# Kernel tuning notes

Hardware: AMD Instinct MI355X
Metric: run time of the kernel (lower is better)

The kernel has to match this reference:

```python
import jax, jax.numpy as jnp
import numpy as np

T, N, E, F_IN, H_GNN, H_OUT, RH, G, C = 8, 10000, 160000, 128, 128, 128, 128, 32, 10


def gcn_layer(x, src, dst, W, b):
    # PyG GCNConv: h = D^-1/2 (A+I) D^-1/2 (x W) + b, self-loops added, edge weight 1
    h = x @ W  # [N, H]
    ones = jnp.ones((E,), h.dtype)
    deg = jax.ops.segment_sum(ones, dst, num_segments=N) + 1.0  # +1 for self-loop
    dinv = jax.lax.rsqrt(deg)
    coef = dinv[src] * dinv[dst]  # [E]
    agg = jax.ops.segment_sum(h[src] * coef[:, None], dst, num_segments=N)
    agg = agg + h * (dinv * dinv)[:, None]  # self-loop term
    return agg + b


def snapshot_encode(x, edge_index, batch, W1, b1, W2, b2):
    src, dst = edge_index[0], edge_index[1]
    h = jax.nn.relu(gcn_layer(x, src, dst, W1, b1))
    h = jax.nn.relu(gcn_layer(h, src, dst, W2, b2))
    sums = jax.ops.segment_sum(h, batch, num_segments=G)  # global_mean_pool
    cnts = jax.ops.segment_sum(jnp.ones((N,), h.dtype), batch, num_segments=G)
    return sums / jnp.maximum(cnts, 1.0)[:, None]  # [G, H_OUT]


def gru_layer(seq, Wih, Whh, bih, bhh):
    # seq: [T, G, in]; torch nn.GRU cell equations
    H = Whh.shape[1]

    def step(h, xt):
        gi = xt @ Wih.T + bih
        gh = h @ Whh.T + bhh
        ir, iz, inn = jnp.split(gi, 3, axis=-1)
        hr, hz, hn = jnp.split(gh, 3, axis=-1)
        r = jax.nn.sigmoid(ir + hr)
        z = jax.nn.sigmoid(iz + hz)
        n = jnp.tanh(inn + r * hn)
        h_new = (1.0 - z) * n + z * h
        return h_new, h_new

    h0 = jnp.zeros((seq.shape[1], H), seq.dtype)
    hT, outs = jax.lax.scan(step, h0, seq)
    return outs, hT


def setup_inputs() -> dict:
    key = jax.random.key(0)
    ks = jax.random.split(key, 20)
    s = 0.05
    inp = {
        "x": jax.random.normal(ks[0], (T, N, F_IN), jnp.float32),
        "edge_index": jax.random.randint(ks[1], (T, 2, E), 0, N),
        "batch": jax.random.randint(ks[2], (T, N), 0, G),
        "W1": jax.random.normal(ks[3], (F_IN, H_GNN), jnp.float32) * s,
        "b1": jnp.zeros((H_GNN,), jnp.float32),
        "W2": jax.random.normal(ks[4], (H_GNN, H_OUT), jnp.float32) * s,
        "b2": jnp.zeros((H_OUT,), jnp.float32),
        "Wih0": jax.random.normal(ks[5], (3 * RH, H_OUT), jnp.float32) * s,
        "Whh0": jax.random.normal(ks[6], (3 * RH, RH), jnp.float32) * s,
        "bih0": jnp.zeros((3 * RH,), jnp.float32),
        "bhh0": jnp.zeros((3 * RH,), jnp.float32),
        "Wih1": jax.random.normal(ks[7], (3 * RH, RH), jnp.float32) * s,
        "Whh1": jax.random.normal(ks[8], (3 * RH, RH), jnp.float32) * s,
        "bih1": jnp.zeros((3 * RH,), jnp.float32),
        "bhh1": jnp.zeros((3 * RH,), jnp.float32),
        "Wc": jax.random.normal(ks[9], (C, RH), jnp.float32) * s,
        "bc": jnp.zeros((C,), jnp.float32),
    }
    return inp


def reference(x, edge_index, batch, W1, b1, W2, b2, Wih0, Whh0, bih0, bhh0,
              Wih1, Whh1, bih1, bhh1, Wc, bc):
    # per-snapshot GNN encode, vmapped over T snapshots -> [T, G, H_OUT]
    emb = jax.vmap(snapshot_encode, in_axes=(0, 0, 0, None, None, None, None))(
        x, edge_index, batch, W1, b1, W2, b2)
    outs, _ = gru_layer(emb, Wih0, Whh0, bih0, bhh0)
    _, hT = gru_layer(outs, Wih1, Whh1, bih1, bhh1)  # h_n[-1]: last layer final state
    return hT @ Wc.T + bc  # [G, C]
```

## Files before the change

kernel.cpp:

```cpp
#include <hip/hip_runtime.h>

#define T_ 8
#define N_ 10000
#define E_ 160000
#define G_ 32
#define C_ 10
#define F_ 128

typedef _Float16 f16;
typedef _Float16 f16x2 __attribute__((ext_vector_type(2)));
typedef _Float16 f16x4 __attribute__((ext_vector_type(4)));
typedef _Float16 f16x8 __attribute__((ext_vector_type(8)));
typedef float floatx4 __attribute__((ext_vector_type(4)));

static constexpr size_t ROWS = (size_t)T_ * N_;
static constexpr int SLICE = E_ / 8;

static constexpr size_t OFF_XH    = 0;
static constexpr size_t OFF_A1    = 20480000;
static constexpr size_t OFF_H1    = 40960000;
static constexpr size_t OFF_REC   = 61440000;
static constexpr size_t OFF_CNT   = 66560000;
static constexpr size_t OFF_DINV  = 69120000;
static constexpr size_t OFF_RP    = 69440000;
static constexpr size_t OFF_CNTG  = 69760032;
static constexpr size_t OFF_BRP   = 69761056;
static constexpr size_t OFF_WP    = 69762112;
static constexpr size_t OFF_BLIST = 69827648;
static constexpr size_t OFF_EMBH  = 70147648;
static constexpr size_t OFF_GPACK = 70213184;
static constexpr size_t OFF_GI0   = 70606400;
static constexpr size_t OFF_PART  = 70999616;

__device__ __forceinline__ float sig_fast(float x) {
  return __builtin_amdgcn_rcpf(1.0f + __builtin_amdgcn_exp2f(-1.4426950408889634f * x));
}
__device__ __forceinline__ float tanh_fast(float x) {
  return 1.0f - 2.0f * __builtin_amdgcn_rcpf(1.0f + __builtin_amdgcn_exp2f(2.8853900817779268f * x));
}

__global__ __launch_bounds__(1024) void hist_kernel(const int* __restrict__ ei,
                                                    const int* __restrict__ batch,
                                                    int* __restrict__ cnt,
                                                    int* __restrict__ cntG) {
  __shared__ int hL[N_];
  __shared__ int cL[G_];
  int b = blockIdx.x, tid = threadIdx.x;
  int t = b & 7, s = b >> 3;
  for (int i = tid; i < N_; i += 1024) hL[i] = 0;
  if (tid < G_) cL[tid] = 0;
  __syncthreads();
  const int* dstp = ei + (size_t)t * 2 * E_ + E_ + s * SLICE;
  for (int e4 = tid; e4 < SLICE / 4; e4 += 1024) {
    int4 d = *(const int4*)(dstp + e4 * 4);
    atomicAdd(&hL[d.x], 1); atomicAdd(&hL[d.y], 1);
    atomicAdd(&hL[d.z], 1); atomicAdd(&hL[d.w], 1);
  }
  if (s == 0)
    for (int n = tid; n < N_; n += 1024) atomicAdd(&cL[batch[t * N_ + n]], 1);
  __syncthreads();
  int* cp = cnt + ((size_t)t * 8 + s) * N_;
  for (int i = tid; i < N_; i += 1024) cp[i] = hL[i];
  if (s == 0 && tid < G_) cntG[t * G_ + tid] = cL[tid];
}

__global__ __launch_bounds__(1024) void scan_kernel(int* __restrict__ cnt,
                                                    int* __restrict__ rp,
                                                    float* __restrict__ dinv,
                                                    const int* __restrict__ cntG,
                                                    int* __restrict__ brp) {
  __shared__ int wsum[16];
  __shared__ int carry;
  int t = blockIdx.x, tid = threadIdx.x, lane = tid & 63, wid = tid >> 6;
  if (t == 8) {
    int v = (tid < 256) ? cntG[tid] : 0;
    for (int ofs = 1; ofs < 64; ofs <<= 1) {
      int u = __shfl_up(v, ofs);
      if (lane >= ofs) v += u;
    }
    if (lane == 63 && wid < 4) wsum[wid] = v;
    __syncthreads();
    if (tid < 256) {
      int base = 0;
      for (int w = 0; w < wid; ++w) base += wsum[w];
      if (tid == 0) brp[0] = 0;
      brp[tid + 1] = v + base;
    }
    return;
  }
  if (tid == 0) { carry = 0; rp[t * (N_ + 1)] = 0; }
  __syncthreads();
  for (int c0 = 0; c0 < N_; c0 += 1024) {
    int n = c0 + tid;
    int vs[8];
    int deg = 0;
    if (n < N_) {
#pragma unroll
      for (int s = 0; s < 8; ++s) {
        vs[s] = cnt[((size_t)t * 8 + s) * N_ + n];
        deg += vs[s];
      }
      dinv[t * N_ + n] = rsqrtf((float)deg + 1.0f);
    }
    int v = (n < N_) ? deg : 0;
    int v0 = v;
    for (int ofs = 1; ofs < 64; ofs <<= 1) {
      int u = __shfl_up(v, ofs);
      if (lane >= ofs) v += u;
    }
    if (lane == 63) wsum[wid] = v;
    __syncthreads();
    if (wid == 0) {
      int w = (lane < 16) ? wsum[lane] : 0;
      for (int ofs = 1; ofs < 16; ofs <<= 1) {
        int u = __shfl_up(w, ofs);
        if (lane >= ofs) w += u;
      }
      if (lane < 16) wsum[lane] = w;
    }
    __syncthreads();
    int base = carry + (wid ? wsum[wid - 1] : 0);
    if (n < N_) {
      rp[t * (N_ + 1) + n + 1] = base + v;
      int run = base + v - v0;
#pragma unroll
      for (int s = 0; s < 8; ++s) {
        int vv = vs[s];
        cnt[((size_t)t * 8 + s) * N_ + n] = run;
        run += vv;
      }
    }
    __syncthreads();
    if (tid == 0) carry += wsum[15];
    __syncthreads();
  }
}

__global__ __launch_bounds__(1024) void fill_kernel(const int* __restrict__ ei,
                                                    const int* __restrict__ base,
                                                    int* __restrict__ rec,
                                                    const int* __restrict__ batch,
                                                    const int* __restrict__ brp,
                                                    int* __restrict__ blist) {
  __shared__ int offL[N_];
  __shared__ int cb[G_];
  int b = blockIdx.x, tid = threadIdx.x;
  int t = b & 7, s = b >> 3;
  const int* bp = base + ((size_t)t * 8 + s) * N_;
  for (int i = tid; i < N_; i += 1024) offL[i] = bp[i];
  if (s == 0 && tid < G_) cb[tid] = brp[t * G_ + tid];
  __syncthreads();
  const int* srcp = ei + (size_t)t * 2 * E_ + s * SLICE;
  const int* dstp = srcp + E_;
  int* rt = rec + (size_t)t * E_;
  for (int e4 = tid; e4 < SLICE / 4; e4 += 1024) {
    int4 sv = *(const int4*)(srcp + e4 * 4);
    int4 dv = *(const int4*)(dstp + e4 * 4);
    int p0 = atomicAdd(&offL[dv.x], 1);
    int p1 = atomicAdd(&offL[dv.y], 1);
    int p2 = atomicAdd(&offL[dv.z], 1);
    int p3 = atomicAdd(&offL[dv.w], 1);
    rt[p0] = sv.x; rt[p1] = sv.y; rt[p2] = sv.z; rt[p3] = sv.w;
  }
  if (s == 0) {
    for (int n = tid; n < N_; n += 1024) {
      int g = batch[t * N_ + n];
      int p = atomicAdd(&cb[g], 1);
      blist[p] = t * N_ + n;
    }
  }
}

__global__ void cvt_kernel(const float* __restrict__ x, const float* __restrict__ dinv,
                           f16* __restrict__ xh) {
  size_t i = ((size_t)blockIdx.x * 256 + threadIdx.x) * 4;
  float4 v = *(const float4*)(x + i);
  float d = dinv[i >> 7];
  f16x4 o; o.x = (f16)(v.x * d); o.y = (f16)(v.y * d);
  o.z = (f16)(v.z * d); o.w = (f16)(v.w * d);
  *(f16x4*)(xh + i) = o;
}

__global__ void agg_kernel(const f16* __restrict__ X, f16* __restrict__ A,
                           const int* __restrict__ rp, const int* __restrict__ rec,
                           const float* __restrict__ dinv) {
  int wave = threadIdx.x >> 6, lane = threadIdx.x & 63;
  int b = blockIdx.x;
  int t = b & 7, i = b >> 3;
  int n = i * 4 + wave;
  int row = t * N_ + n;
  float ds = dinv[row];
  f16x2 xv = *(const f16x2*)(X + (size_t)row * F_ + 2 * lane);
  float a00 = (float)xv.x, a01 = (float)xv.y;
  float a10 = 0.f, a11 = 0.f, a20 = 0.f, a21 = 0.f, a30 = 0.f, a31 = 0.f;
  int beg = rp[t * (N_ + 1) + n], end = rp[t * (N_ + 1) + n + 1];
  beg = __builtin_amdgcn_readfirstlane(beg);
  end = __builtin_amdgcn_readfirstlane(end);
  const int* rc = rec + (size_t)t * E_;
  const f16* Xt = X + (size_t)t * N_ * F_;
  int e = beg;
  int i0 = 0, i1 = 0, i2 = 0, i3 = 0;
  if (e + 3 < end) { i0 = rc[e]; i1 = rc[e + 1]; i2 = rc[e + 2]; i3 = rc[e + 3]; }
  for (; e + 7 < end; e += 4) {
    int n0 = rc[e + 4], n1 = rc[e + 5], n2 = rc[e + 6], n3 = rc[e + 7];
    f16x2 h0 = *(const f16x2*)(Xt + (size_t)i0 * F_ + 2 * lane);
    f16x2 h1 = *(const f16x2*)(Xt + (size_t)i1 * F_ + 2 * lane);
    f16x2 h2 = *(const f16x2*)(Xt + (size_t)i2 * F_ + 2 * lane);
    f16x2 h3 = *(const f16x2*)(Xt + (size_t)i3 * F_ + 2 * lane);
    a00 += (float)h0.x; a01 += (float)h0.y;
    a10 += (float)h1.x; a11 += (float)h1.y;
    a20 += (float)h2.x; a21 += (float)h2.y;
    a30 += (float)h3.x; a31 += (float)h3.y;
    i0 = n0; i1 = n1; i2 = n2; i3 = n3;
  }
  if (e + 3 < end) {
    f16x2 h0 = *(const f16x2*)(Xt + (size_t)i0 * F_ + 2 * lane);
    f16x2 h1 = *(const f16x2*)(Xt + (size_t)i1 * F_ + 2 * lane);
    f16x2 h2 = *(const f16x2*)(Xt + (size_t)i2 * F_ + 2 * lane);
    f16x2 h3 = *(const f16x2*)(Xt + (size_t)i3 * F_ + 2 * lane);
    a00 += (float)h0.x; a01 += (float)h0.y;
    a10 += (float)h1.x; a11 += (float)h1.y;
    a20 += (float)h2.x; a21 += (float)h2.y;
    a30 += (float)h3.x; a31 += (float)h3.y;
    e += 4;
  }
  for (; e < end; ++e) {
    int s = rc[e];
    f16x2 hv = *(const f16x2*)(Xt + (size_t)s * F_ + 2 * lane);
    a00 += (float)hv.x; a01 += (float)hv.y;
  }
  float r0 = ds * ((a00 + a10) + (a20 + a30));
  float r1 = ds * ((a01 + a11) + (a21 + a31));
  f16x2 o; o.x = (f16)r0; o.y = (f16)r1;
  *(f16x2*)(A + (size_t)row * F_ + 2 * lane) = o;
}

__global__ void packall_kernel(const float* __restrict__ W1, const float* __restrict__ W2,
                               f16* __restrict__ Wp,
                               const float* __restrict__ A0, const float* __restrict__ A1,
                               const float* __restrict__ A2, const float* __restrict__ A3,
                               f16* __restrict__ gp) {
  int idx = blockIdx.x * 256 + threadIdx.x;
  if (idx < 32768) {
    const float* W = (idx < 16384) ? W1 : W2;
    int l = idx & 16383;
    int j = l & 7, lane = (l >> 3) & 63, ct = (l >> 9) & 7, kc = (l >> 12) & 3;
    int k = kc * 32 + ((lane >> 4) & 3) * 8 + j;
    int n = ct * 16 + (lane & 15);
    Wp[idx] = (f16)W[k * 128 + n];
  } else {
    int gidx = idx - 32768;
    int mat = gidx / 49152, l = gidx - mat * 49152;
    int j = l & 7, lane = (l >> 3) & 63, kc = (l >> 9) & 3, nt = l >> 11;
    int k = kc * 32 + ((lane >> 4) & 3) * 8 + j;
    int u = nt * 16 + (lane & 15);
    const float* W = (mat == 0) ? A0 : (mat == 1) ? A1 : (mat == 2) ? A2 : A3;
    gp[gidx] = (f16)W[u * 128 + k];
  }
}

__global__ __launch_bounds__(256) void gemm_kernel(const f16* __restrict__ A,
                                                   const f16* __restrict__ Wp,
                                                   const float* __restrict__ bias,
                                                   const float* __restrict__ scale,
                                                   f16* __restrict__ O) {
  __shared__ f16x8 Bp[2048];
  const f16x8* Wv = (const f16x8*)Wp;
  for (int i = threadIdx.x; i < 2048; i += 256) Bp[i] = Wv[i];
  __syncthreads();
  int wave = threadIdx.x >> 6, lane = threadIdx.x & 63;
  int quad = lane >> 4, m = lane & 15;
  int rowbase = blockIdx.x * 64 + wave * 16;
  const f16x8* Arow = (const f16x8*)(A + (size_t)(rowbase + m) * F_);
  floatx4 acc[8];
#pragma unroll
  for (int ct = 0; ct < 8; ++ct) { floatx4 z = {0.f, 0.f, 0.f, 0.f}; acc[ct] = z; }
#pragma unroll
  for (int kc = 0; kc < 4; ++kc) {
    f16x8 a = Arow[kc * 4 + quad];
#pragma unroll
    for (int ct = 0; ct < 8; ++ct)
      acc[ct] = __builtin_amdgcn_mfma_f32_16x16x32_f16(a, Bp[(kc * 8 + ct) * 64 + lane],
                                                       acc[ct], 0, 0, 0);
  }
  float sv[4];
#pragma unroll
  for (int r = 0; r < 4; ++r)
    sv[r] = scale ? scale[rowbase + quad * 4 + r] : 1.0f;
#pragma unroll
  for (int ct = 0; ct < 8; ++ct) {
    int colc = ct * 16 + m;
    float bv = bias[colc];
#pragma unroll
    for (int r = 0; r < 4; ++r) {
      int row = rowbase + quad * 4 + r;
      float v = fmaxf(acc[ct][r] + bv, 0.0f) * sv[r];
      O[(size_t)row * F_ + colc] = (f16)v;
    }
  }
}

__global__ void pool1_kernel(const f16* __restrict__ H, const int* __restrict__ brp,
                             const int* __restrict__ blist, float* __restrict__ part) {
  int b = blockIdx.x;
  int wave = threadIdx.x >> 6, lane = threadIdx.x & 63;
  int idx = b >> 1;
  int s = (b & 1) * 4 + wave;
  int beg = brp[idx], end = brp[idx + 1];
  beg = __builtin_amdgcn_readfirstlane(beg);
  end = __builtin_amdgcn_readfirstlane(end);
  int len = end - beg;
  int lo = beg + (int)(((long long)len * s) >> 3);
  int hi = beg + (int)(((long long)len * (s + 1)) >> 3);
  float a00 = 0.f, a01 = 0.f, a10 = 0.f, a11 = 0.f;
  float a20 = 0.f, a21 = 0.f, a30 = 0.f, a31 = 0.f;
  int e = lo;
  for (; e + 3 < hi; e += 4) {
    int r0 = blist[e], r1 = blist[e + 1], r2 = blist[e + 2], r3 = blist[e + 3];
    f16x2 v0 = *(const f16x2*)(H + (size_t)r0 * F_ + 2 * lane);
    f16x2 v1 = *(const f16x2*)(H + (size_t)r1 * F_ + 2 * lane);
    f16x2 v2 = *(const f16x2*)(H + (size_t)r2 * F_ + 2 * lane);
    f16x2 v3 = *(const f16x2*)(H + (size_t)r3 * F_ + 2 * lane);
    a00 += (float)v0.x; a01 += (float)v0.y;
    a10 += (float)v1.x; a11 += (float)v1.y;
    a20 += (float)v2.x; a21 += (float)v2.y;
    a30 += (float)v3.x; a31 += (float)v3.y;
  }
  for (; e < hi; ++e) {
    int r = blist[e];
    f16x2 v = *(const f16x2*)(H + (size_t)r * F_ + 2 * lane);
    a00 += (float)v.x; a01 += (float)v.y;
  }
  float2 o;
  o.x = (a00 + a10) + (a20 + a30);
  o.y = (a01 + a11) + (a21 + a31);
  *(float2*)(part + ((size_t)idx * 8 + s) * F_ + 2 * lane) = o;
}

__global__ void pool2_kernel(const float* __restrict__ part, const int* __restrict__ brp,
                             f16* __restrict__ embh) {
  int idx = blockIdx.x * 2 + (threadIdx.x >> 7);
  int f = threadIdx.x & 127;
  float s = 0.f;
#pragma unroll
  for (int k = 0; k < 8; ++k) s += part[((size_t)idx * 8 + k) * F_ + f];
  int cnt = brp[idx + 1] - brp[idx];
  embh[(size_t)idx * F_ + f] = (f16)(s / fmaxf((float)cnt, 1.0f));
}

__global__ __launch_bounds__(256) void gi0_kernel(const f16* __restrict__ embh,
                                                  const f16* __restrict__ gp,
                                                  float* __restrict__ gi0) {
  int wave = threadIdx.x >> 6, lane = threadIdx.x & 63;
  int quad = lane >> 4, mm = lane & 15;
  int rowbase = blockIdx.x * 64 + wave * 16;
  const f16* Arow = embh + (size_t)(rowbase + mm) * 128;
  floatx4 acc[24];
#pragma unroll
  for (int nt = 0; nt < 24; ++nt) { floatx4 z = {0.f, 0.f, 0.f, 0.f}; acc[nt] = z; }
#pragma unroll
  for (int kc = 0; kc < 4; ++kc) {
    f16x8 a = *(const f16x8*)(Arow + kc * 32 + quad * 8);
#pragma unroll
    for (int nt = 0; nt < 24; ++nt) {
      f16x8 b = *(const f16x8*)(gp + (size_t)(((nt * 4 + kc) * 64 + lane)) * 8);
      acc[nt] = __builtin_amdgcn_mfma_f32_16x16x32_f16(a, b, acc[nt], 0, 0, 0);
    }
  }
#pragma unroll
  for (int nt = 0; nt < 24; ++nt)
#pragma unroll
    for (int r = 0; r < 4; ++r)
      gi0[(size_t)(rowbase + quad * 4 + r) * 384 + nt * 16 + mm] = acc[nt][r];
}

__global__ __launch_bounds__(256, 1) void gru_fused(
    const f16* __restrict__ gp, const float* __restrict__ gi0,
    const float* __restrict__ bih0, const float* __restrict__ bhh0,
    const float* __restrict__ bih1, const float* __restrict__ bhh1,
    const float* __restrict__ Wc, const float* __restrict__ bc,
    float* __restrict__ out) {
  __shared__ f16 hb0[16 * 136];
  __shared__ f16 hb1[16 * 136];
  __shared__ float ghb[2 * 384];
  __shared__ float gib[2 * 384];
  __shared__ float h1s[2 * 128];
  int tid = threadIdx.x, wave = tid >> 6, lane = tid & 63;
  int quad = lane >> 4, mm = lane & 15;
  int g2 = tid >> 7, f = tid & 127;
  int bid = blockIdx.x;

  f16x8 B0[24], B1[24];
#pragma unroll
  for (int i = 0; i < 6; ++i)
#pragma unroll
    for (int kc = 0; kc < 4; ++kc) {
      size_t off = (size_t)((((wave * 6 + i) * 4 + kc) * 64 + lane)) * 8;
      B0[i * 4 + kc] = *(const f16x8*)(gp + 1 * 49152 + off);
      B1[i * 4 + kc] = *(const f16x8*)(gp + 3 * 49152 + off);
    }
  float br0 = bih0[f] + bhh0[f];
  float bz0 = bih0[128 + f] + bhh0[128 + f];
  float bni0 = bih0[256 + f], bnh0 = bhh0[256 + f];
  float br1 = bih1[f] + bhh1[f];
  float bz1 = bih1[128 + f] + bhh1[128 + f];
  float bni1 = bih1[256 + f], bnh1 = bhh1[256 + f];

  for (int i = tid; i < 16 * 136; i += 256) { hb0[i] = (f16)0.f; hb1[i] = (f16)0.f; }
  float h0 = 0.f, h1 = 0.f;
  __syncthreads();

  const f16* wih1 = gp + 2 * 49152;
  for (int t = 0; t < T_; ++t) {
    f16x8 Bs[24];
#pragma unroll
    for (int i = 0; i < 6; ++i)
#pragma unroll
      for (int kc = 0; kc < 4; ++kc)
        Bs[i * 4 + kc] = *(const f16x8*)(wih1 +
            (size_t)((((wave * 6 + i) * 4 + kc) * 64 + lane)) * 8);
    const float* gi = gi0 + (size_t)(t * G_ + bid * 2 + g2) * 384;
    float gir = gi[f], giz = gi[128 + f], gin = gi[256 + f];

    floatx4 acc[6];
#pragma unroll
    for (int i = 0; i < 6; ++i) { floatx4 z = {0.f, 0.f, 0.f, 0.f}; acc[i] = z; }
#pragma unroll
    for (int kc = 0; kc < 4; ++kc) {
      f16x8 a = *(const f16x8*)(hb0 + mm * 136 + kc * 32 + quad * 8);
#pragma unroll
      for (int i = 0; i < 6; ++i)
        acc[i] = __builtin_amdgcn_mfma_f32_16x16x32_f16(a, B0[i * 4 + kc], acc[i], 0, 0, 0);
    }
    if (quad == 0) {
#pragma unroll
      for (int i = 0; i < 6; ++i) {
        ghb[0 * 384 + wave * 96 + i * 16 + mm] = acc[i][0];
        ghb[1 * 384 + wave * 96 + i * 16 + mm] = acc[i][1];
      }
    }
    __syncthreads();

    {
      float hr = ghb[g2 * 384 + f];
      float hz = ghb[g2 * 384 + 128 + f];
      float hn = ghb[g2 * 384 + 256 + f];
      float r = sig_fast(gir + hr + br0);
      float z = sig_fast(giz + hz + bz0);
      float nn = tanh_fast(gin + bni0 + r * (hn + bnh0));
      h0 = (1.0f - z) * nn + z * h0;
      hb0[g2 * 136 + f] = (f16)h0;
    }
    __syncthreads();

    floatx4 accx[6], acch[6];
#pragma unroll
    for (int i = 0; i < 6; ++i) {
      floatx4 z = {0.f, 0.f, 0.f, 0.f}; accx[i] = z; acch[i] = z;
    }
#pragma unroll
    for (int kc = 0; kc < 4; ++kc) {
      f16x8 ax = *(const f16x8*)(hb0 + mm * 136 + kc * 32 + quad * 8);
      f16x8 ah = *(const f16x8*)(hb1 + mm * 136 + kc * 32 + quad * 8);
#pragma unroll
      for (int i = 0; i < 6; ++i) {
        accx[i] = __builtin_amdgcn_mfma_f32_16x16x32_f16(ax, Bs[i * 4 + kc], accx[i], 0, 0, 0);
        acch[i] = __builtin_amdgcn_mfma_f32_16x16x32_f16(ah, B1[i * 4 + kc], acch[i], 0, 0, 0);
      }
    }
    if (quad == 0) {
#pragma unroll
      for (int i = 0; i < 6; ++i) {
        gib[0 * 384 + wave * 96 + i * 16 + mm] = accx[i][0];
        gib[1 * 384 + wave * 96 + i * 16 + mm] = accx[i][1];
        ghb[0 * 384 + wave * 96 + i * 16 + mm] = acch[i][0];
        ghb[1 * 384 + wave * 96 + i * 16 + mm] = acch[i][1];
      }
    }
    __syncthreads();

    {
      float i1r = gib[g2 * 384 + f];
      float i1z = gib[g2 * 384 + 128 + f];
      float i1n = gib[g2 * 384 + 256 + f];
      float hr = ghb[g2 * 384 + f];
      float hz = ghb[g2 * 384 + 128 + f];
      float hn = ghb[g2 * 384 + 256 + f];
      float r = sig_fast(i1r + hr + br1);
      float z = sig_fast(i1z + hz + bz1);
      float nn = tanh_fast(i1n + bni1 + r * (hn + bnh1));
      h1 = (1.0f - z) * nn + z * h1;
      hb1[g2 * 136 + f] = (f16)h1;
    }
    __syncthreads();
  }

  h1s[g2 * 128 + f] = h1;
  __syncthreads();
  if (tid < 2 * C_) {
    int gg = tid / C_, c = tid - gg * C_;
    float s = bc[c];
    const float* wr = Wc + (size_t)c * 128;
    const float* hr = h1s + gg * 128;
    for (int k = 0; k < 128; k += 4) {
      float4 w = *(const float4*)(wr + k);
      s += hr[k] * w.x + hr[k + 1] * w.y + hr[k + 2] * w.z + hr[k + 3] * w.w;
    }
    out[(bid * 2 + gg) * C_ + c] = s;
  }
}

extern "C" void kernel_launch(void* const* d_in, const int* in_sizes, int n_in,
                              void* d_out, int out_size, void* d_ws, size_t ws_size,
                              hipStream_t stream) {
  const float* x    = (const float*)d_in[0];
  const int*   ei   = (const int*)d_in[1];
  const int*   batch= (const int*)d_in[2];
  const float* W1   = (const float*)d_in[3];
  const float* b1   = (const float*)d_in[4];
  const float* W2   = (const float*)d_in[5];
  const float* b2   = (const float*)d_in[6];
  const float* Wih0 = (const float*)d_in[7];
  const float* Whh0 = (const float*)d_in[8];
  const float* bih0 = (const float*)d_in[9];
  const float* bhh0 = (const float*)d_in[10];
  const float* Wih1 = (const float*)d_in[11];
  const float* Whh1 = (const float*)d_in[12];
  const float* bih1 = (const float*)d_in[13];
  const float* bhh1 = (const float*)d_in[14];
  const float* Wc   = (const float*)d_in[15];
  const float* bc   = (const float*)d_in[16];
  float* out = (float*)d_out;

  char* ws = (char*)d_ws;
  f16*   Xh    = (f16*)(ws + OFF_XH);
  f16*   A1    = (f16*)(ws + OFF_A1);
  f16*   H1    = (f16*)(ws + OFF_H1);
  f16*   A2    = A1;
  f16*   H2    = Xh;
  int*   rec   = (int*)(ws + OFF_REC);
  int*   cnt   = (int*)(ws + OFF_CNT);
  float* dinv  = (float*)(ws + OFF_DINV);
  int*   rp    = (int*)(ws + OFF_RP);
  int*   cntG  = (int*)(ws + OFF_CNTG);
  int*   brp   = (int*)(ws + OFF_BRP);
  f16*   Wp    = (f16*)(ws + OFF_WP);
  int*   blist = (int*)(ws + OFF_BLIST);
  f16*   embh  = (f16*)(ws + OFF_EMBH);
  f16*   gp    = (f16*)(ws + OFF_GPACK);
  float* gi0   = (float*)(ws + OFF_GI0);
  float* part  = (float*)(ws + OFF_PART);

  packall_kernel<<<896, 256, 0, stream>>>(W1, W2, Wp, Wih0, Whh0, Wih1, Whh1, gp);
  hist_kernel<<<64, 1024, 0, stream>>>(ei, batch, cnt, cntG);
  scan_kernel<<<9, 1024, 0, stream>>>(cnt, rp, dinv, cntG, brp);
  cvt_kernel<<<10000, 256, 0, stream>>>(x, dinv, Xh);
  fill_kernel<<<64, 1024, 0, stream>>>(ei, cnt, rec, batch, brp, blist);

  agg_kernel<<<20000, 256, 0, stream>>>(Xh, A1, rp, rec, dinv);
  gemm_kernel<<<1250, 256, 0, stream>>>(A1, Wp, b1, dinv, H1);
  agg_kernel<<<20000, 256, 0, stream>>>(H1, A2, rp, rec, dinv);
  gemm_kernel<<<1250, 256, 0, stream>>>(A2, Wp + 16384, b2, (const float*)nullptr, H2);

  pool1_kernel<<<512, 256, 0, stream>>>(H2, brp, blist, part);
  pool2_kernel<<<128, 256, 0, stream>>>(part, brp, embh);
  gi0_kernel<<<4, 256, 0, stream>>>(embh, gp, gi0);
  gru_fused<<<16, 256, 0, stream>>>(gp, gi0, bih0, bhh0, bih1, bhh1, Wc, bc, out);
}
```

Baseline: 309.3 us.

## Fuse neighbor aggregation with the dense GEMM in each GCN layer

Merges the separate agg and gemm kernels into one kernel per layer. Each block first gathers 64 aggregated rows into shared memory, then runs the MFMA GEMM with bias, ReLU and scaling straight from that shared tile. This removes the round-trip of the intermediate aggregated buffer through global memory and drops it from the workspace. In exchange each wave now walks 16 rows one after another with far fewer blocks, and shared memory use per block rises. That can reduce how many gather loads are in flight and lower occupancy.

```diff
diff --git a/kernel.cpp b/kernel.cpp
--- a/kernel.cpp
+++ b/kernel.cpp
@@ -17,20 +17,19 @@
 static constexpr int SLICE = E_ / 8;
 
 static constexpr size_t OFF_XH    = 0;
-static constexpr size_t OFF_A1    = 20480000;
-static constexpr size_t OFF_H1    = 40960000;
-static constexpr size_t OFF_REC   = 61440000;
-static constexpr size_t OFF_CNT   = 66560000;
-static constexpr size_t OFF_DINV  = 69120000;
-static constexpr size_t OFF_RP    = 69440000;
-static constexpr size_t OFF_CNTG  = 69760032;
-static constexpr size_t OFF_BRP   = 69761056;
-static constexpr size_t OFF_WP    = 69762112;
-static constexpr size_t OFF_BLIST = 69827648;
-static constexpr size_t OFF_EMBH  = 70147648;
-static constexpr size_t OFF_GPACK = 70213184;
-static constexpr size_t OFF_GI0   = 70606400;
-static constexpr size_t OFF_PART  = 70999616;
+static constexpr size_t OFF_H1    = 20480000;
+static constexpr size_t OFF_REC   = 40960000;
+static constexpr size_t OFF_CNT   = 46080000;
+static constexpr size_t OFF_DINV  = 48640000;
+static constexpr size_t OFF_RP    = 48960000;
+static constexpr size_t OFF_CNTG  = 49280032;
+static constexpr size_t OFF_BRP   = 49281056;
+static constexpr size_t OFF_WP    = 49282112;
+static constexpr size_t OFF_BLIST = 49347648;
+static constexpr size_t OFF_EMBH  = 49667648;
+static constexpr size_t OFF_GPACK = 49733184;
+static constexpr size_t OFF_GI0   = 50126400;
+static constexpr size_t OFF_PART  = 50519616;
 
 __device__ __forceinline__ float sig_fast(float x) {
   return __builtin_amdgcn_rcpf(1.0f + __builtin_amdgcn_exp2f(-1.4426950408889634f * x));
@@ -181,58 +180,104 @@
   *(f16x4*)(xh + i) = o;
 }
 
-__global__ void agg_kernel(const f16* __restrict__ X, f16* __restrict__ A,
-                           const int* __restrict__ rp, const int* __restrict__ rec,
-                           const float* __restrict__ dinv) {
-  int wave = threadIdx.x >> 6, lane = threadIdx.x & 63;
-  int b = blockIdx.x;
-  int t = b & 7, i = b >> 3;
-  int n = i * 4 + wave;
-  int row = t * N_ + n;
-  float ds = dinv[row];
-  f16x2 xv = *(const f16x2*)(X + (size_t)row * F_ + 2 * lane);
-  float a00 = (float)xv.x, a01 = (float)xv.y;
-  float a10 = 0.f, a11 = 0.f, a20 = 0.f, a21 = 0.f, a30 = 0.f, a31 = 0.f;
-  int beg = rp[t * (N_ + 1) + n], end = rp[t * (N_ + 1) + n + 1];
-  beg = __builtin_amdgcn_readfirstlane(beg);
-  end = __builtin_amdgcn_readfirstlane(end);
+__global__ __launch_bounds__(256) void agg_gemm_kernel(
+    const f16* __restrict__ X, const int* __restrict__ rp, const int* __restrict__ rec,
+    const float* __restrict__ dinv, const f16* __restrict__ Wp,
+    const float* __restrict__ bias, const float* __restrict__ scale,
+    f16* __restrict__ O) {
+  __shared__ f16 At[64 * 136];
+  __shared__ f16x8 Bp[2048];
+  int tid = threadIdx.x, wave = tid >> 6, lane = tid & 63;
+  const f16x8* Wv = (const f16x8*)Wp;
+  for (int i = tid; i < 2048; i += 256) Bp[i] = Wv[i];
+  int b = blockIdx.x, t = b & 7, ib = b >> 3;
+  const int* rpt = rp + t * (N_ + 1);
   const int* rc = rec + (size_t)t * E_;
   const f16* Xt = X + (size_t)t * N_ * F_;
-  int e = beg;
-  int i0 = 0, i1 = 0, i2 = 0, i3 = 0;
-  if (e + 3 < end) { i0 = rc[e]; i1 = rc[e + 1]; i2 = rc[e + 2]; i3 = rc[e + 3]; }
-  for (; e + 7 < end; e += 4) {
-    int n0 = rc[e + 4], n1 = rc[e + 5], n2 = rc[e + 6], n3 = rc[e + 7];
-    f16x2 h0 = *(const f16x2*)(Xt + (size_t)i0 * F_ + 2 * lane);
-    f16x2 h1 = *(const f16x2*)(Xt + (size_t)i1 * F_ + 2 * lane);
-    f16x2 h2 = *(const f16x2*)(Xt + (size_t)i2 * F_ + 2 * lane);
-    f16x2 h3 = *(const f16x2*)(Xt + (size_t)i3 * F_ + 2 * lane);
-    a00 += (float)h0.x; a01 += (float)h0.y;
-    a10 += (float)h1.x; a11 += (float)h1.y;
-    a20 += (float)h2.x; a21 += (float)h2.y;
-    a30 += (float)h3.x; a31 += (float)h3.y;
-    i0 = n0; i1 = n1; i2 = n2; i3 = n3;
-  }
-  if (e + 3 < end) {
-    f16x2 h0 = *(const f16x2*)(Xt + (size_t)i0 * F_ + 2 * lane);
-    f16x2 h1 = *(const f16x2*)(Xt + (size_t)i1 * F_ + 2 * lane);
-    f16x2 h2 = *(const f16x2*)(Xt + (size_t)i2 * F_ + 2 * lane);
-    f16x2 h3 = *(const f16x2*)(Xt + (size_t)i3 * F_ + 2 * lane);
-    a00 += (float)h0.x; a01 += (float)h0.y;
-    a10 += (float)h1.x; a11 += (float)h1.y;
-    a20 += (float)h2.x; a21 += (float)h2.y;
-    a30 += (float)h3.x; a31 += (float)h3.y;
-    e += 4;
-  }
-  for (; e < end; ++e) {
-    int s = rc[e];
-    f16x2 hv = *(const f16x2*)(Xt + (size_t)s * F_ + 2 * lane);
-    a00 += (float)hv.x; a01 += (float)hv.y;
-  }
-  float r0 = ds * ((a00 + a10) + (a20 + a30));
-  float r1 = ds * ((a01 + a11) + (a21 + a31));
-  f16x2 o; o.x = (f16)r0; o.y = (f16)r1;
-  *(f16x2*)(A + (size_t)row * F_ + 2 * lane) = o;
+  for (int m = 0; m < 16; ++m) {
+    int rl = wave * 16 + m;
+    int n = ib * 64 + rl;
+    f16x2 o;
+    if (n < N_) {
+      float ds = dinv[t * N_ + n];
+      f16x2 xv = *(const f16x2*)(Xt + (size_t)n * F_ + 2 * lane);
+      float a00 = (float)xv.x, a01 = (float)xv.y;
+      float a10 = 0.f, a11 = 0.f, a20 = 0.f, a21 = 0.f, a30 = 0.f, a31 = 0.f;
+      int beg = rpt[n], end = rpt[n + 1];
+      beg = __builtin_amdgcn_readfirstlane(beg);
+      end = __builtin_amdgcn_readfirstlane(end);
+      int e = beg;
+      int i0 = 0, i1 = 0, i2 = 0, i3 = 0;
+      if (e + 3 < end) { i0 = rc[e]; i1 = rc[e + 1]; i2 = rc[e + 2]; i3 = rc[e + 3]; }
+      for (; e + 7 < end; e += 4) {
+        int n0 = rc[e + 4], n1 = rc[e + 5], n2 = rc[e + 6], n3 = rc[e + 7];
+        f16x2 h0 = *(const f16x2*)(Xt + (size_t)i0 * F_ + 2 * lane);
+        f16x2 h1 = *(const f16x2*)(Xt + (size_t)i1 * F_ + 2 * lane);
+        f16x2 h2 = *(const f16x2*)(Xt + (size_t)i2 * F_ + 2 * lane);
+        f16x2 h3 = *(const f16x2*)(Xt + (size_t)i3 * F_ + 2 * lane);
+        a00 += (float)h0.x; a01 += (float)h0.y;
+        a10 += (float)h1.x; a11 += (float)h1.y;
+        a20 += (float)h2.x; a21 += (float)h2.y;
+        a30 += (float)h3.x; a31 += (float)h3.y;
+        i0 = n0; i1 = n1; i2 = n2; i3 = n3;
+      }
+      if (e + 3 < end) {
+        f16x2 h0 = *(const f16x2*)(Xt + (size_t)i0 * F_ + 2 * lane);
+        f16x2 h1 = *(const f16x2*)(Xt + (size_t)i1 * F_ + 2 * lane);
+        f16x2 h2 = *(const f16x2*)(Xt + (size_t)i2 * F_ + 2 * lane);
+        f16x2 h3 = *(const f16x2*)(Xt + (size_t)i3 * F_ + 2 * lane);
+        a00 += (float)h0.x; a01 += (float)h0.y;
+        a10 += (float)h1.x; a11 += (float)h1.y;
+        a20 += (float)h2.x; a21 += (float)h2.y;
+        a30 += (float)h3.x; a31 += (float)h3.y;
+        e += 4;
+      }
+      for (; e < end; ++e) {
+        int s = rc[e];
+        f16x2 hv = *(const f16x2*)(Xt + (size_t)s * F_ + 2 * lane);
+        a00 += (float)hv.x; a01 += (float)hv.y;
+      }
+      o.x = (f16)(ds * ((a00 + a10) + (a20 + a30)));
+      o.y = (f16)(ds * ((a01 + a11) + (a21 + a31)));
+    } else {
+      o.x = (f16)0.f; o.y = (f16)0.f;
+    }
+    *(f16x2*)(At + rl * 136 + 2 * lane) = o;
+  }
+  __syncthreads();
+  int quad = lane >> 4, mm = lane & 15;
+  const f16* Arow = At + (wave * 16 + mm) * 136;
+  floatx4 acc[8];
+#pragma unroll
+  for (int ct = 0; ct < 8; ++ct) { floatx4 z = {0.f, 0.f, 0.f, 0.f}; acc[ct] = z; }
+#pragma unroll
+  for (int kc = 0; kc < 4; ++kc) {
+    f16x8 a = *(const f16x8*)(Arow + kc * 32 + quad * 8);
+#pragma unroll
+    for (int ct = 0; ct < 8; ++ct)
+      acc[ct] = __builtin_amdgcn_mfma_f32_16x16x32_f16(a, Bp[(kc * 8 + ct) * 64 + lane],
+                                                       acc[ct], 0, 0, 0);
+  }
+  float sv[4];
+  int nbase = ib * 64 + wave * 16 + quad * 4;
+#pragma unroll
+  for (int r = 0; r < 4; ++r) {
+    int n = nbase + r;
+    sv[r] = (scale && n < N_) ? scale[t * N_ + n] : 1.0f;
+  }
+#pragma unroll
+  for (int ct = 0; ct < 8; ++ct) {
+    int colc = ct * 16 + mm;
+    float bv = bias[colc];
+#pragma unroll
+    for (int r = 0; r < 4; ++r) {
+      int n = nbase + r;
+      if (n < N_) {
+        float v = fmaxf(acc[ct][r] + bv, 0.0f) * sv[r];
+        O[((size_t)t * N_ + n) * F_ + colc] = (f16)v;
+      }
+    }
+  }
 }
 
 __global__ void packall_kernel(const float* __restrict__ W1, const float* __restrict__ W2,
@@ -256,47 +301,6 @@
     int u = nt * 16 + (lane & 15);
     const float* W = (mat == 0) ? A0 : (mat == 1) ? A1 : (mat == 2) ? A2 : A3;
     gp[gidx] = (f16)W[u * 128 + k];
-  }
-}
-
-__global__ __launch_bounds__(256) void gemm_kernel(const f16* __restrict__ A,
-                                                   const f16* __restrict__ Wp,
-                                                   const float* __restrict__ bias,
-                                                   const float* __restrict__ scale,
-                                                   f16* __restrict__ O) {
-  __shared__ f16x8 Bp[2048];
-  const f16x8* Wv = (const f16x8*)Wp;
-  for (int i = threadIdx.x; i < 2048; i += 256) Bp[i] = Wv[i];
-  __syncthreads();
-  int wave = threadIdx.x >> 6, lane = threadIdx.x & 63;
-  int quad = lane >> 4, m = lane & 15;
-  int rowbase = blockIdx.x * 64 + wave * 16;
-  const f16x8* Arow = (const f16x8*)(A + (size_t)(rowbase + m) * F_);
-  floatx4 acc[8];
-#pragma unroll
-  for (int ct = 0; ct < 8; ++ct) { floatx4 z = {0.f, 0.f, 0.f, 0.f}; acc[ct] = z; }
-#pragma unroll
-  for (int kc = 0; kc < 4; ++kc) {
-    f16x8 a = Arow[kc * 4 + quad];
-#pragma unroll
-    for (int ct = 0; ct < 8; ++ct)
-      acc[ct] = __builtin_amdgcn_mfma_f32_16x16x32_f16(a, Bp[(kc * 8 + ct) * 64 + lane],
-                                                       acc[ct], 0, 0, 0);
-  }
-  float sv[4];
-#pragma unroll
-  for (int r = 0; r < 4; ++r)
-    sv[r] = scale ? scale[rowbase + quad * 4 + r] : 1.0f;
-#pragma unroll
-  for (int ct = 0; ct < 8; ++ct) {
-    int colc = ct * 16 + m;
-    float bv = bias[colc];
-#pragma unroll
-    for (int r = 0; r < 4; ++r) {
-      int row = rowbase + quad * 4 + r;
-      float v = fmaxf(acc[ct][r] + bv, 0.0f) * sv[r];
-      O[(size_t)row * F_ + colc] = (f16)v;
-    }
   }
 }
 
@@ -534,9 +538,7 @@
 
   char* ws = (char*)d_ws;
   f16*   Xh    = (f16*)(ws + OFF_XH);
-  f16*   A1    = (f16*)(ws + OFF_A1);
   f16*   H1    = (f16*)(ws + OFF_H1);
-  f16*   A2    = A1;
   f16*   H2    = Xh;
   int*   rec   = (int*)(ws + OFF_REC);
   int*   cnt   = (int*)(ws + OFF_CNT);
@@ -557,10 +559,9 @@
   cvt_kernel<<<10000, 256, 0, stream>>>(x, dinv, Xh);
   fill_kernel<<<64, 1024, 0, stream>>>(ei, cnt, rec, batch, brp, blist);
 
-  agg_kernel<<<20000, 256, 0, stream>>>(Xh, A1, rp, rec, dinv);
-  gemm_kernel<<<1250, 256, 0, stream>>>(A1, Wp, b1, dinv, H1);
-  agg_kernel<<<20000, 256, 0, stream>>>(H1, A2, rp, rec, dinv);
-  gemm_kernel<<<1250, 256, 0, stream>>>(A2, Wp + 16384, b2, (const float*)nullptr, H2);
+  agg_gemm_kernel<<<1256, 256, 0, stream>>>(Xh, rp, rec, dinv, Wp, b1, dinv, H1);
+  agg_gemm_kernel<<<1256, 256, 0, stream>>>(H1, rp, rec, dinv, Wp + 16384, b2,
+                                            (const float*)nullptr, H2);
 
   pool1_kernel<<<512, 256, 0, stream>>>(H2, brp, blist, part);
   pool2_kernel<<<128, 256, 0, stream>>>(part, brp, embh);
```

Measured after the change: 369.3 us. +19.4%, slower.
